# Performance work log

Hardware: AMD Instinct MI355X
Metric: run time of the kernel (lower is better)

The kernel has to match this reference:

```python
import jax, jax.numpy as jnp
import numpy as np

EPS = 1e-8


def setup_inputs() -> dict:
    key = jax.random.key(0)
    ks = jax.random.split(key, 3)
    B, d_in, d_sae = 2048, 2048, 16384
    x = jax.random.normal(ks[0], (B, 2, d_in), dtype=jnp.float32)
    W_enc = jax.random.normal(ks[1], (d_in, d_sae), dtype=jnp.float32) / (d_in ** 0.5)
    W_dec = jax.random.normal(ks[2], (d_sae, d_in), dtype=jnp.float32) / (d_sae ** 0.5)
    b_enc = jnp.zeros((d_sae,), dtype=jnp.float32)
    b_dec = jnp.zeros((d_in,), dtype=jnp.float32)
    return {"x": x, "W_enc": W_enc, "W_dec": W_dec, "b_enc": b_enc,
            "b_dec": b_dec, "k": 64, "h": 8192}


def _encode(x, W_enc, b_enc, k):
    # x: (N, d_in) -> z: (N, d_sae), top-k sparsified with relu on kept values
    pre = x @ W_enc + b_enc
    v, i = jax.lax.top_k(pre, k)                       # (N, k)
    rows = jnp.arange(pre.shape[0])[:, None]
    return jnp.zeros_like(pre).at[rows, i].set(jax.nn.relu(v))


def _info_nce(z_a, z_b):
    z_a = z_a / jnp.maximum(jnp.linalg.norm(z_a, axis=-1, keepdims=True), EPS)
    z_b = z_b / jnp.maximum(jnp.linalg.norm(z_b, axis=-1, keepdims=True), EPS)
    sim = z_a @ z_b.T                                  # (B, B)
    diag = jnp.diagonal(sim)
    ce_row = jnp.mean(jax.nn.logsumexp(sim, axis=1) - diag)
    ce_col = jnp.mean(jax.nn.logsumexp(sim, axis=0) - diag)
    return 0.5 * (ce_row + ce_col)


def reference(x, W_enc, W_dec, b_enc, b_dec, k, h):
    alpha = 1.0
    B, _, d_in = x.shape
    # encode both tokens in one GEMM: (2B, d_in)
    x_flat = x.reshape(B * 2, d_in)
    z = _encode(x_flat, W_enc, b_enc, k)               # (2B, d_sae)
    x_hat_full = z @ W_dec + b_dec                     # (2B, d_in)
    x_hat_high = z[:, :h] @ W_dec[:h, :] + b_dec       # (2B, d_in)
    per_tok = d_in
    # mean over batch per token, summed over prev+cur (matches 4 separate means)
    se_full = jnp.sum((x_hat_full - x_flat) ** 2, axis=-1).reshape(B, 2)
    se_high = jnp.sum((x_hat_high - x_flat) ** 2, axis=-1).reshape(B, 2)
    l_matr = (jnp.mean(se_full, axis=0).sum() + jnp.mean(se_high, axis=0).sum()) / per_tok
    z2 = z.reshape(B, 2, -1)
    z_h_prev = z2[:, 0, :h]
    z_h_cur = z2[:, 1, :h]
    l_contr = _info_nce(z_h_cur, z_h_prev)
    total = l_matr + alpha * l_contr
    x_hat_cur = x_hat_full.reshape(B, 2, d_in)[:, 1]
    z_cur = z2[:, 1]
    return (total, x_hat_cur, z_cur)
```

## Files before the change

kernel.cpp:

```cpp
#include <hip/hip_runtime.h>
#include <hip/hip_bf16.h>
#include <math.h>

#define D_IN   2048
#define D_SAE  16384
#define NROWS  4096
#define KTOP   64
#define HDIM   8192
#define CHUNK  1024
#define EPSN   1e-8f
#define BANDW_F16 4e-3f
#define BANDW_F32 4e-4f
#define BANDCAP 512
#define NTILE   128
#define SEG     16
#define CAPT    (NTILE*SEG)
#define TH_CAND 2.0f

typedef unsigned short u16;
typedef unsigned char u8;
typedef _Float16 f16;
typedef __attribute__((ext_vector_type(8))) _Float16 f16x8;
typedef __attribute__((ext_vector_type(4))) _Float16 f16x4;
typedef __attribute__((ext_vector_type(8))) unsigned short u16x8;
typedef __attribute__((ext_vector_type(4))) float float4v;
typedef __attribute__((ext_vector_type(2))) float f32x2;

__device__ __forceinline__ unsigned f2u(float f) {
  unsigned b = __float_as_uint(f);
  return (b & 0x80000000u) ? ~b : (b | 0x80000000u);
}
__device__ __forceinline__ float u2f(unsigned u) {
  unsigned b = (u & 0x80000000u) ? (u & 0x7fffffffu) : ~u;
  return __uint_as_float(b);
}
__device__ __forceinline__ u16 f2bf_rne(float f) {
  unsigned b = __float_as_uint(f);
  unsigned r = (b + 0x7fffu + ((b >> 16) & 1u)) >> 16;
  return (u16)r;
}
__device__ __forceinline__ float bf2f(u16 u) {
  return __uint_as_float(((unsigned)u) << 16);
}
__device__ __forceinline__ void async_copy16(void* lds, const void* g) {
  __builtin_amdgcn_global_load_lds(
      (const __attribute__((address_space(1))) unsigned*)(g),
      (__attribute__((address_space(3))) unsigned*)(lds), 16, 0, 0);
}

__global__ __launch_bounds__(256)
void pre_kernel(const float* __restrict__ x, const float* __restrict__ W,
                f16* __restrict__ Axh, f16* __restrict__ Th,
                float* __restrict__ WT)
{
  __shared__ float S[64][65];
  const int bid = blockIdx.x;
  if (bid < 8192) {
    const int tx = threadIdx.x & 63, ty = threadIdx.x >> 6;
    const int n0 = (bid & 255) * 64, k0 = (bid >> 8) * 64;
#pragma unroll
    for (int i = 0; i < 16; ++i) {
      int kl = ty + i * 4;
      S[kl][tx] = W[(size_t)(k0 + kl) * D_SAE + n0 + tx];
    }
    __syncthreads();
#pragma unroll
    for (int i = 0; i < 16; ++i) {
      int nl = ty + i * 4;
      float v = S[tx][nl];
      Th[(size_t)(n0 + nl) * D_IN + k0 + tx] = (f16)v;
      WT[(size_t)(n0 + nl) * D_IN + k0 + tx] = v;
    }
  } else {
    int t = (bid - 8192) * 256 + threadIdx.x;
    const int n4 = (NROWS * D_IN) / 4;
    if (t < n4) {
      float4 v = ((const float4*)x)[t];
      f16x4 h;
      h.x = (f16)v.x; h.y = (f16)v.y; h.z = (f16)v.z; h.w = (f16)v.w;
      ((f16x4*)Axh)[t] = h;
    }
  }
}

__global__ __launch_bounds__(256)
void wdec_to_fp8_kernel(const float* __restrict__ W,
                        u8* __restrict__ W8, float* __restrict__ scl)
{
  __shared__ float red[256];
  const int c = blockIdx.x;
  const int tid = threadIdx.x;
  const int e0 = tid * 8;
  const float* wr = W + (size_t)c * 2048;
  float4 a = *(const float4*)(wr + e0);
  float4 b = *(const float4*)(wr + e0 + 4);
  float w[8] = {a.x,a.y,a.z,a.w,b.x,b.y,b.z,b.w};
  float mx = 0.f;
#pragma unroll
  for (int i = 0; i < 8; ++i) mx = fmaxf(mx, fabsf(w[i]));
  red[tid] = mx; __syncthreads();
  for (int s = 128; s > 0; s >>= 1) { if (tid < s) red[tid] = fmaxf(red[tid], red[tid+s]); __syncthreads(); }
  const float mxa = red[0];
  const float senc = mxa > 0.f ? 448.f / mxa : 0.f;
  float q[8];
#pragma unroll
  for (int i = 0; i < 8; ++i) q[i] = fminf(fmaxf(w[i] * senc, -448.f), 448.f);
  int p0 = __builtin_amdgcn_cvt_pk_fp8_f32(q[0], q[1], 0, false);
  p0 = __builtin_amdgcn_cvt_pk_fp8_f32(q[2], q[3], p0, true);
  int p1 = __builtin_amdgcn_cvt_pk_fp8_f32(q[4], q[5], 0, false);
  p1 = __builtin_amdgcn_cvt_pk_fp8_f32(q[6], q[7], p1, true);
  uint2 o; o.x = (unsigned)p0; o.y = (unsigned)p1;
  *(uint2*)(W8 + (size_t)c * 2048 + e0) = o;
  if (tid == 0) scl[c] = mxa > 0.f ? mxa / 448.f : 0.f;
}

__global__ __launch_bounds__(512, 2)
void gemm_f16_kernel(const f16* __restrict__ Axh,
                     const f16* __restrict__ BT,
                     const float* __restrict__ bias,
                     unsigned* __restrict__ ckey_g,
                     u16* __restrict__ cidx_g,
                     unsigned* __restrict__ ccnt)
{
  __shared__ u16 As[2][2][256 * 32];
  __shared__ u16 Bs[2][2][256 * 32];
  const int tid  = threadIdx.x;
  const int wave = tid >> 6, lane = tid & 63;
  const int bid  = blockIdx.x;
  const int xcd  = bid & 7, loc = bid >> 3;
  const int n0   = (xcd * 8 + (loc >> 4)) * 256;
  const int m0   = (loc & 15) * 256;
  const int wr   = wave >> 2;
  const int wc   = wave & 3;
  const int fr   = lane & 15;
  const int fsl  = lane >> 4;

  float4v acc[8][4];
#pragma unroll
  for (int i = 0; i < 8; ++i)
#pragma unroll
    for (int j = 0; j < 4; ++j) acc[i][j] = (float4v){0.f, 0.f, 0.f, 0.f};

  int aoff[8], boff[4];
#pragma unroll
  for (int mi = 0; mi < 8; ++mi) {
    int row = wr * 128 + mi * 16 + fr;
    aoff[mi] = row * 32 + ((fsl ^ ((row >> 1) & 3)) * 8);
  }
#pragma unroll
  for (int n = 0; n < 4; ++n) {
    int col = wc * 64 + n * 16 + fr;
    boff[n] = col * 32 + ((fsl ^ ((col >> 1) & 3)) * 8);
  }

  auto stA = [&](int bf, int tt, int ks, int half) {
    int idx = half * 512 + tid;
    int row = idx >> 2, sl = idx & 3;
    int gc = tt * 64 + ks * 32 + ((sl ^ ((row >> 1) & 3)) * 8);
    async_copy16((char*)&As[bf][ks][0] + (size_t)idx * 16,
                 Axh + (size_t)(m0 + row) * D_IN + gc);
  };
  auto stB = [&](int bf, int tt, int ks, int half) {
    int idx = half * 512 + tid;
    int row = idx >> 2, sl = idx & 3;
    int gc = tt * 64 + ks * 32 + ((sl ^ ((row >> 1) & 3)) * 8);
    async_copy16((char*)&Bs[bf][ks][0] + (size_t)idx * 16,
                 BT + (size_t)(n0 + row) * D_IN + gc);
  };

  stA(0, 0, 0, 0); stA(0, 0, 0, 1); stB(0, 0, 0, 0); stB(0, 0, 0, 1);
  stA(0, 0, 1, 0); stA(0, 0, 1, 1); stB(0, 0, 1, 0); stB(0, 0, 1, 1);
  asm volatile("s_waitcnt vmcnt(4)" ::: "memory");
  __builtin_amdgcn_s_barrier();

  for (int t = 0; t < 32; ++t) {
    const int buf = t & 1, nbf = buf ^ 1;
    const bool st = (t < 31);
#pragma unroll
    for (int ks = 0; ks < 2; ++ks) {
      const u16* Ak = &As[buf][ks][0];
      const u16* Bk = &Bs[buf][ks][0];
      f16x8 b0 = *(const f16x8*)&Bk[boff[0]];
      f16x8 b1 = *(const f16x8*)&Bk[boff[1]];
      f16x8 b2 = *(const f16x8*)&Bk[boff[2]];
      f16x8 b3 = *(const f16x8*)&Bk[boff[3]];
      f16x8 a0 = *(const f16x8*)&Ak[aoff[0]];
      f16x8 a1 = *(const f16x8*)&Ak[aoff[1]];
      f16x8 a2 = *(const f16x8*)&Ak[aoff[2]];
      f16x8 a3 = *(const f16x8*)&Ak[aoff[3]];
      if (st) { stA(nbf, t + 1, ks, 0); stA(nbf, t + 1, ks, 1); }
      __builtin_amdgcn_s_setprio(1);
      acc[0][0] = __builtin_amdgcn_mfma_f32_16x16x32_f16(a0, b0, acc[0][0], 0, 0, 0);
      acc[0][1] = __builtin_amdgcn_mfma_f32_16x16x32_f16(a0, b1, acc[0][1], 0, 0, 0);
      acc[0][2] = __builtin_amdgcn_mfma_f32_16x16x32_f16(a0, b2, acc[0][2], 0, 0, 0);
      acc[0][3] = __builtin_amdgcn_mfma_f32_16x16x32_f16(a0, b3, acc[0][3], 0, 0, 0);
      acc[1][0] = __builtin_amdgcn_mfma_f32_16x16x32_f16(a1, b0, acc[1][0], 0, 0, 0);
      acc[1][1] = __builtin_amdgcn_mfma_f32_16x16x32_f16(a1, b1, acc[1][1], 0, 0, 0);
      acc[1][2] = __builtin_amdgcn_mfma_f32_16x16x32_f16(a1, b2, acc[1][2], 0, 0, 0);
      acc[1][3] = __builtin_amdgcn_mfma_f32_16x16x32_f16(a1, b3, acc[1][3], 0, 0, 0);
      acc[2][0] = __builtin_amdgcn_mfma_f32_16x16x32_f16(a2, b0, acc[2][0], 0, 0, 0);
      acc[2][1] = __builtin_amdgcn_mfma_f32_16x16x32_f16(a2, b1, acc[2][1], 0, 0, 0);
      acc[2][2] = __builtin_amdgcn_mfma_f32_16x16x32_f16(a2, b2, acc[2][2], 0, 0, 0);
      acc[2][3] = __builtin_amdgcn_mfma_f32_16x16x32_f16(a2, b3, acc[2][3], 0, 0, 0);
      acc[3][0] = __builtin_amdgcn_mfma_f32_16x16x32_f16(a3, b0, acc[3][0], 0, 0, 0);
      acc[3][1] = __builtin_amdgcn_mfma_f32_16x16x32_f16(a3, b1, acc[3][1], 0, 0, 0);
      acc[3][2] = __builtin_amdgcn_mfma_f32_16x16x32_f16(a3, b2, acc[3][2], 0, 0, 0);
      acc[3][3] = __builtin_amdgcn_mfma_f32_16x16x32_f16(a3, b3, acc[3][3], 0, 0, 0);
      __builtin_amdgcn_s_setprio(0);
      a0 = *(const f16x8*)&Ak[aoff[4]];
      a1 = *(const f16x8*)&Ak[aoff[5]];
      a2 = *(const f16x8*)&Ak[aoff[6]];
      a3 = *(const f16x8*)&Ak[aoff[7]];
      if (st) { stB(nbf, t + 1, ks, 0); stB(nbf, t + 1, ks, 1); }
      __builtin_amdgcn_s_setprio(1);
      acc[4][0] = __builtin_amdgcn_mfma_f32_16x16x32_f16(a0, b0, acc[4][0], 0, 0, 0);
      acc[4][1] = __builtin_amdgcn_mfma_f32_16x16x32_f16(a0, b1, acc[4][1], 0, 0, 0);
      acc[4][2] = __builtin_amdgcn_mfma_f32_16x16x32_f16(a0, b2, acc[4][2], 0, 0, 0);
      acc[4][3] = __builtin_amdgcn_mfma_f32_16x16x32_f16(a0, b3, acc[4][3], 0, 0, 0);
      acc[5][0] = __builtin_amdgcn_mfma_f32_16x16x32_f16(a1, b0, acc[5][0], 0, 0, 0);
      acc[5][1] = __builtin_amdgcn_mfma_f32_16x16x32_f16(a1, b1, acc[5][1], 0, 0, 0);
      acc[5][2] = __builtin_amdgcn_mfma_f32_16x16x32_f16(a1, b2, acc[5][2], 0, 0, 0);
      acc[5][3] = __builtin_amdgcn_mfma_f32_16x16x32_f16(a1, b3, acc[5][3], 0, 0, 0);
      acc[6][0] = __builtin_amdgcn_mfma_f32_16x16x32_f16(a2, b0, acc[6][0], 0, 0, 0);
      acc[6][1] = __builtin_amdgcn_mfma_f32_16x16x32_f16(a2, b1, acc[6][1], 0, 0, 0);
      acc[6][2] = __builtin_amdgcn_mfma_f32_16x16x32_f16(a2, b2, acc[6][2], 0, 0, 0);
      acc[6][3] = __builtin_amdgcn_mfma_f32_16x16x32_f16(a2, b3, acc[6][3], 0, 0, 0);
      acc[7][0] = __builtin_amdgcn_mfma_f32_16x16x32_f16(a3, b0, acc[7][0], 0, 0, 0);
      acc[7][1] = __builtin_amdgcn_mfma_f32_16x16x32_f16(a3, b1, acc[7][1], 0, 0, 0);
      acc[7][2] = __builtin_amdgcn_mfma_f32_16x16x32_f16(a3, b2, acc[7][2], 0, 0, 0);
      acc[7][3] = __builtin_amdgcn_mfma_f32_16x16x32_f16(a3, b3, acc[7][3], 0, 0, 0);
      __builtin_amdgcn_s_setprio(0);
      if (st) {
        asm volatile("s_waitcnt vmcnt(4)" ::: "memory");
        __builtin_amdgcn_s_barrier();
      } else if (ks == 0) {
        asm volatile("s_waitcnt vmcnt(0)" ::: "memory");
        __builtin_amdgcn_s_barrier();
      }
    }
  }
  __syncthreads();

  unsigned* lcnt = (unsigned*)&As[0][0][0];
  lcnt[tid] = 0u;
  __syncthreads();
  const int tl = wc >> 1;
  const int tileG = (n0 >> 7) + tl;
  const int orow = (lane >> 4) * 4;
#pragma unroll
  for (int mi = 0; mi < 8; ++mi) {
#pragma unroll
    for (int nj = 0; nj < 4; ++nj) {
      int col = n0 + wc * 64 + nj * 16 + fr;
      float bv = bias[col];
#pragma unroll
      for (int rr = 0; rr < 4; ++rr) {
        float val = acc[mi][nj][rr] + bv;
        if (val >= TH_CAND) {
          int lrow = wr * 128 + mi * 16 + orow + rr;
          unsigned j = atomicAdd(&lcnt[tl * 256 + lrow], 1u);
          if (j < SEG) {
            size_t sb = ((size_t)(m0 + lrow) * NTILE + tileG) * SEG;
            ckey_g[sb + j] = f2u(val);
            cidx_g[sb + j] = (u16)col;
          }
        }
      }
    }
  }
  __syncthreads();
  ccnt[(size_t)(m0 + (tid & 255)) * NTILE + (n0 >> 7) + (tid >> 8)] = lcnt[tid];
}

__global__ __launch_bounds__(256)
void select_compact_kernel(const unsigned* __restrict__ ckey_g,
                           const u16* __restrict__ cidx_g,
                           const unsigned* __restrict__ ccnt,
                           const float* __restrict__ x,
                           const float* __restrict__ WT,
                           const float* __restrict__ benc,
                           float bandw,
                           int*   __restrict__ topk_idx,
                           float* __restrict__ topk_val,
                           float* __restrict__ nh_norm,
                           unsigned* __restrict__ flags)
{
  __shared__ unsigned ckey[CAPT];
  __shared__ u16      cidx[CAPT];
  __shared__ unsigned tof[128];
  __shared__ unsigned tc[128];
  __shared__ unsigned hist[256];
  __shared__ unsigned sscan[257];
  __shared__ unsigned wsum[4];
  __shared__ float    bv_l[64];
  __shared__ int      band_idx[BANDCAP];
  __shared__ float    band_val[BANDCAP];
  __shared__ double   band_ex[BANDCAP];
  __shared__ unsigned char picked[BANDCAP];
  __shared__ int      out_idx[64];
  __shared__ float    out_val[64];
  __shared__ float    sh_v64;
  __shared__ unsigned sh_mcnt, sh_bstar, sh_kth, sh_ocnt, sh_bcnt, sh_bad;

  const int tid = threadIdx.x;
  const int wv = tid >> 6, ln = tid & 63;
  const int r = blockIdx.x;

  if (tid == 0) { sh_ocnt = 0u; sh_bcnt = 0u; sh_bad = 0u; sh_mcnt = 0u; sh_bstar = 0xffffffffu; }
  hist[tid] = 0u;
  if (tid < 128) {
    unsigned c = ccnt[(size_t)r * NTILE + tid];
    tc[tid] = c;
    if (c > SEG) sh_bad = 1u;
  }
  __syncthreads();
  if (tid < 128) {
    unsigned v = tc[tid];
#pragma unroll
    for (int d = 1; d < 64; d <<= 1) {
      unsigned t = __shfl_up(v, d);
      if (ln >= d) v += t;
    }
    tof[tid] = v;
  }
  __syncthreads();
  if (tid >= 64 && tid < 128) tof[tid] += tof[63];
  __syncthreads();
  const unsigned cc_u = tof[127];
  const int cc = (int)(cc_u < CAPT ? cc_u : CAPT);

  {
    unsigned ck[8]; u16 ci[8]; unsigned pv[8];
#pragma unroll
    for (int b = 0; b < 8; ++b) {
      int idx = tid + 256 * b;
      int tile = idx >> 4, slot = idx & 15;
      unsigned c = tc[tile]; if (c > SEG) c = SEG;
      bool valid = (unsigned)slot < c;
      pv[b] = valid ? (tof[tile] - tc[tile] + slot) : 0xffffffffu;
      ck[b] = valid ? ckey_g[(size_t)r * CAPT + idx] : 0u;
      ci[b] = valid ? cidx_g[(size_t)r * CAPT + idx] : (u16)0;
    }
#pragma unroll
    for (int b = 0; b < 8; ++b) {
      if (pv[b] < (unsigned)CAPT) { ckey[pv[b]] = ck[b]; cidx[pv[b]] = ci[b]; }
    }
  }
  __syncthreads();

  bool bad = (sh_bad != 0u) || (cc_u < 64u) || (cc_u > (unsigned)CAPT);

  if (!bad) {
    for (int s = tid; s < cc; s += 256) {
      float v = u2f(ckey[s]);
      int b = (int)((v - TH_CAND) * 100.0f);
      b = b < 0 ? 0 : (b > 255 ? 255 : b);
      atomicAdd(&hist[b], 1u);
    }
  }
  __syncthreads();
  {
    int rt = 255 - tid;
    unsigned v = hist[rt];
#pragma unroll
    for (int d = 1; d < 64; d <<= 1) {
      unsigned t = __shfl_up(v, d);
      if (ln >= d) v += t;
    }
    if (ln == 63) wsum[wv] = v;
    __syncthreads();
    unsigned add = 0;
    for (int w = 0; w < wv; ++w) add += wsum[w];
    sscan[rt] = v + add;
    if (tid == 0) sscan[256] = 0u;
    __syncthreads();
    if (sscan[tid] >= 64u && sscan[tid + 1] < 64u) {
      sh_bstar = (unsigned)tid;
      sh_kth = 64u - sscan[tid + 1];
    }
  }
  __syncthreads();

  if (bad || sh_bstar == 0xffffffffu) { if (tid == 0) flags[r] = 1u; return; }
  const int bstar = (int)sh_bstar;
  const unsigned kth = sh_kth;

  for (int s = tid; s < cc; s += 256) {
    float v = u2f(ckey[s]);
    int b = (int)((v - TH_CAND) * 100.0f);
    b = b < 0 ? 0 : (b > 255 ? 255 : b);
    if (b == bstar) {
      unsigned p = atomicAdd(&sh_mcnt, 1u);
      if (p < 64u) bv_l[p] = v;
    }
  }
  __syncthreads();
  if (sh_mcnt > 64u) { if (tid == 0) flags[r] = 1u; return; }
  const int m = (int)sh_mcnt;
  if (wv == 0 && ln < m) {
    float mine = bv_l[ln];
    int rank = 0;
    for (int j = 0; j < m; ++j) {
      float o = bv_l[j];
      if (o > mine || (o == mine && j < ln)) ++rank;
    }
    if (rank == (int)kth - 1) sh_v64 = mine;
  }
  __syncthreads();
  const float v64 = sh_v64;

  const float hi = v64 + 2.f * bandw, lo = v64 - 2.f * bandw;
  for (int s = tid; s < cc; s += 256) {
    float v = u2f(ckey[s]);
    int i = (int)cidx[s];
    if (v > hi) {
      unsigned p = atomicAdd(&sh_ocnt, 1u);
      out_idx[p] = i; out_val[p] = v;
    } else if (v >= lo) {
      unsigned p = atomicAdd(&sh_bcnt, 1u);
      if (p < BANDCAP) { band_idx[p] = i; band_val[p] = v; }
    }
  }
  __syncthreads();
  if (sh_bcnt > BANDCAP) { if (tid == 0) flags[r] = 1u; return; }
  const unsigned nci = sh_ocnt;
  const unsigned bcnt = sh_bcnt;
  const unsigned remaining = 64u - nci;

  if (bcnt == remaining) {
    for (unsigned s = tid; s < bcnt; s += 256) {
      out_idx[nci + s] = band_idx[s];
      out_val[nci + s] = band_val[s];
    }
    __syncthreads();
  } else {
    const float* xr = x + (size_t)r * 2048;
    for (unsigned bi = wv; bi < bcnt; bi += 4) {
      int c = band_idx[bi];
      const float* wr = WT + (size_t)c * 2048;
      double s = 0.0;
      for (int j0 = 0; j0 < 2048; j0 += 512) {
        float xa[8], wa[8];
#pragma unroll
        for (int u = 0; u < 8; ++u) {
          int j = j0 + ln + 64 * u;
          xa[u] = xr[j];
          wa[u] = wr[j];
        }
#pragma unroll
        for (int u = 0; u < 8; ++u)
          s += (double)xa[u] * (double)wa[u];
      }
#pragma unroll
      for (int off2 = 32; off2 > 0; off2 >>= 1)
        s += __shfl_down(s, off2);
      if (ln == 0) band_ex[bi] = s + (double)benc[c];
    }
    __syncthreads();
    if (tid == 0) {
      for (unsigned i2 = 0; i2 < bcnt; ++i2) picked[i2] = 0;
      for (unsigned s = 0; s < remaining; ++s) {
        int best = -1;
        for (unsigned b2 = 0; b2 < bcnt; ++b2) {
          if (picked[b2]) continue;
          if (best < 0 || band_ex[b2] > band_ex[best] ||
              (band_ex[b2] == band_ex[best] && band_idx[b2] < band_idx[best]))
            best = (int)b2;
        }
        picked[best] = 1;
        out_idx[nci + s] = band_idx[best];
        out_val[nci + s] = (float)band_ex[best];
      }
    }
    __syncthreads();
  }

  if (tid < 64) {
    float v = out_val[tid];
    v = v > 0.f ? v : 0.f;
    out_val[tid] = v;
    topk_idx[(size_t)r * 64 + tid] = out_idx[tid];
    topk_val[(size_t)r * 64 + tid] = v;
  }
  __syncthreads();
  if (tid == 0) {
    float n2 = 0.f;
    for (int s = 0; s < 64; ++s)
      if (out_idx[s] < HDIM) n2 += out_val[s] * out_val[s];
    nh_norm[r] = sqrtf(n2);
    flags[r] = 0u;
  }
}

__global__ __launch_bounds__(256)
void repair_kernel(const unsigned* __restrict__ flags,
                   const float* __restrict__ x,
                   const float* __restrict__ WT,
                   const float* __restrict__ benc,
                   int* __restrict__ topk_idx,
                   float* __restrict__ topk_val,
                   float* __restrict__ nh_norm)
{
  const int r = blockIdx.x;
  if (flags[r] == 0u) return;
  __shared__ float prerow[16384];
  __shared__ float xs[2048];
  __shared__ float rv[256];
  __shared__ int   ri[256];
  __shared__ int   oi[64];
  __shared__ float ov[64];
  const int tid = threadIdx.x;
  for (int i = tid; i < 2048; i += 256) xs[i] = x[(size_t)r * 2048 + i];
  __syncthreads();
  for (int c = tid; c < 16384; c += 256) {
    const float* wr = WT + (size_t)c * 2048;
    float s = 0.f;
    for (int j = 0; j < 2048; ++j) s = fmaf(xs[j], wr[j], s);
    prerow[c] = s + benc[c];
  }
  __syncthreads();
  for (int k2 = 0; k2 < 64; ++k2) {
    float bv = -INFINITY; int bi = 16384;
    for (int c = tid; c < 16384; c += 256) {
      float v = prerow[c];
      if (v > bv || (v == bv && c < bi)) { bv = v; bi = c; }
    }
    rv[tid] = bv; ri[tid] = bi;
    __syncthreads();
    for (int s2 = 128; s2 > 0; s2 >>= 1) {
      if (tid < s2) {
        if (rv[tid+s2] > rv[tid] || (rv[tid+s2] == rv[tid] && ri[tid+s2] < ri[tid])) {
          rv[tid] = rv[tid+s2]; ri[tid] = ri[tid+s2];
        }
      }
      __syncthreads();
    }
    if (tid == 0) { oi[k2] = ri[0]; ov[k2] = rv[0]; prerow[ri[0]] = -INFINITY; }
    __syncthreads();
  }
  if (tid < 64) {
    float v = ov[tid]; v = v > 0.f ? v : 0.f;
    topk_idx[(size_t)r * 64 + tid] = oi[tid];
    topk_val[(size_t)r * 64 + tid] = v;
  }
  __syncthreads();
  if (tid == 0) {
    float n2 = 0.f;
    for (int s = 0; s < 64; ++s)
      if (oi[s] < HDIM) { float v = ov[s] > 0.f ? ov[s] : 0.f; n2 += v * v; }
    nh_norm[r] = sqrtf(n2);
  }
}

__global__ __launch_bounds__(256)
void scatter_kernel(const int* __restrict__ topk_idx,
                    const float* __restrict__ topk_val,
                    const float* __restrict__ nh_norm,
                    float* __restrict__ zcur_out,
                    u16* __restrict__ ZpTb)
{
  int t = blockIdx.x * blockDim.x + threadIdx.x;
  if (t >= NROWS * 64) return;
  int r = t >> 6;
  int c = topk_idx[t];
  float v = topk_val[t];
  int b = r >> 1;
  if (r & 1) {
    zcur_out[(size_t)b * 16384 + c] = v;
  } else if (c < HDIM) {
    float nrm = nh_norm[r]; nrm = nrm > EPSN ? nrm : EPSN;
    ZpTb[(size_t)c * 2048 + b] = f2bf_rne(v / nrm);
  }
}

__global__ __launch_bounds__(256)
void token_kernel(const int* __restrict__ topk_idx,
                  const float* __restrict__ topk_val,
                  const u8* __restrict__ W8,
                  const float* __restrict__ scl,
                  const float* __restrict__ bdec,
                  const float* __restrict__ x,
                  const float* __restrict__ nh_norm,
                  const u16* __restrict__ ZpTb,
                  float* __restrict__ se_full,
                  float* __restrict__ se_high,
                  float* __restrict__ xhat_out,
                  float* __restrict__ simb,
                  float* __restrict__ lse_row,
                  float* __restrict__ diag)
{
  __shared__ int sidx[64];
  __shared__ float sval[64];
  __shared__ float red[256];
  __shared__ int cidx2[64];
  __shared__ float cval2[64];
  __shared__ int scnt;
  const int tid = threadIdx.x;
  const int r = blockIdx.x;
  const int e0 = tid * 8;
  if (tid == 0) scnt = 0;
  if (tid < 64) {
    int c = topk_idx[(size_t)r*64+tid];
    sidx[tid] = c;
    sval[tid] = topk_val[(size_t)r*64+tid] * scl[c];
  }
  __syncthreads();
  float accf[8], acch[8];
  {
    float4 b0 = *(const float4*)(bdec + e0);
    float4 b1 = *(const float4*)(bdec + e0 + 4);
    accf[0]=b0.x; accf[1]=b0.y; accf[2]=b0.z; accf[3]=b0.w;
    accf[4]=b1.x; accf[5]=b1.y; accf[6]=b1.z; accf[7]=b1.w;
#pragma unroll
    for (int i = 0; i < 8; ++i) acch[i] = accf[i];
  }
  for (int s0 = 0; s0 < 64; s0 += 8) {
    uint2 w[8]; float vf[8], vh[8];
#pragma unroll
    for (int j = 0; j < 8; ++j) {
      int c = sidx[s0 + j];
      float v = sval[s0 + j];
      vf[j] = v;
      vh[j] = (c < HDIM) ? v : 0.f;
      w[j] = *(const uint2*)(W8 + (size_t)c * 2048 + e0);
    }
#pragma unroll
    for (int j = 0; j < 8; ++j) {
      f32x2 f0 = __builtin_amdgcn_cvt_pk_f32_fp8((int)w[j].x, false);
      f32x2 f1 = __builtin_amdgcn_cvt_pk_f32_fp8((int)w[j].x, true);
      f32x2 f2 = __builtin_amdgcn_cvt_pk_f32_fp8((int)w[j].y, false);
      f32x2 f3 = __builtin_amdgcn_cvt_pk_f32_fp8((int)w[j].y, true);
      float wvv[8] = {f0[0],f0[1],f1[0],f1[1],f2[0],f2[1],f3[0],f3[1]};
#pragma unroll
      for (int i = 0; i < 8; ++i) {
        accf[i] = fmaf(vf[j], wvv[i], accf[i]);
        acch[i] = fmaf(vh[j], wvv[i], acch[i]);
      }
    }
  }
  const float* xr = x + (size_t)r * 2048;
  float4 x0 = *(const float4*)(xr + e0);
  float4 x1 = *(const float4*)(xr + e0 + 4);
  float xv[8] = {x0.x,x0.y,x0.z,x0.w,x1.x,x1.y,x1.z,x1.w};
  float sf = 0.f, shs = 0.f;
#pragma unroll
  for (int i = 0; i < 8; ++i) {
    float df = accf[i] - xv[i]; sf += df*df;
    float dh = acch[i] - xv[i]; shs += dh*dh;
  }
  red[tid] = sf; __syncthreads();
  for (int s2=128; s2>0; s2>>=1){ if (tid<s2) red[tid]+=red[tid+s2]; __syncthreads(); }
  if (tid==0) se_full[r] = red[0];
  __syncthreads();
  red[tid] = shs; __syncthreads();
  for (int s2=128; s2>0; s2>>=1){ if (tid<s2) red[tid]+=red[tid+s2]; __syncthreads(); }
  if (tid==0) se_high[r] = red[0];
  if (!(r & 1)) return;

  {
    float* orow = xhat_out + (size_t)(r >> 1) * 2048;
    float4 o0 = {accf[0],accf[1],accf[2],accf[3]};
    float4 o1 = {accf[4],accf[5],accf[6],accf[7]};
    *(float4*)(orow + e0) = o0;
    *(float4*)(orow + e0 + 4) = o1;
  }
  const int i = r >> 1;
  __syncthreads();
  if (tid < 64) {
    int c = sidx[tid];
    float v = topk_val[(size_t)r*64+tid];
    if (c < HDIM) {
      float nrm = nh_norm[r]; nrm = nrm > EPSN ? nrm : EPSN;
      int p = atomicAdd(&scnt, 1);
      cidx2[p] = c; cval2[p] = v / nrm;
    }
  }
  __syncthreads();
  float acc[8];
#pragma unroll
  for (int ii = 0; ii < 8; ++ii) acc[ii] = 0.f;
  const int m = scnt;
  int s = 0;
  for (; s + 8 <= m; s += 8) {
    u16x8 z[8]; float vv[8];
#pragma unroll
    for (int j = 0; j < 8; ++j) {
      vv[j] = cval2[s + j];
      z[j] = *(const u16x8*)(ZpTb + (size_t)cidx2[s + j] * 2048 + e0);
    }
#pragma unroll
    for (int j = 0; j < 8; ++j)
#pragma unroll
      for (int ii = 0; ii < 8; ++ii)
        acc[ii] = fmaf(vv[j], bf2f(z[j][ii]), acc[ii]);
  }
  for (; s < m; ++s) {
    int c = cidx2[s]; float v = cval2[s];
    u16x8 z8 = *(const u16x8*)(ZpTb + (size_t)c * 2048 + e0);
#pragma unroll
    for (int ii = 0; ii < 8; ++ii)
      acc[ii] = fmaf(v, bf2f(z8[ii]), acc[ii]);
  }
  {
    float* srow = simb + (size_t)i * 2048;
    float4 o0 = {acc[0],acc[1],acc[2],acc[3]};
    float4 o1 = {acc[4],acc[5],acc[6],acc[7]};
    *(float4*)(srow + e0) = o0;
    *(float4*)(srow + e0 + 4) = o1;
  }
  float mx = -INFINITY;
#pragma unroll
  for (int ii = 0; ii < 8; ++ii) mx = fmaxf(mx, acc[ii]);
  if ((i >> 3) == tid) diag[i] = acc[i & 7];
  red[tid] = mx; __syncthreads();
  for (int s2=128; s2>0; s2>>=1){ if (tid<s2) red[tid]=fmaxf(red[tid],red[tid+s2]); __syncthreads(); }
  mx = red[0]; __syncthreads();
  float se = 0.f;
#pragma unroll
  for (int ii = 0; ii < 8; ++ii) se += expf(acc[ii] - mx);
  red[tid] = se; __syncthreads();
  for (int s2=128; s2>0; s2>>=1){ if (tid<s2) red[tid]+=red[tid+s2]; __syncthreads(); }
  if (tid == 0) lse_row[i] = mx + logf(red[0]);
}

__global__ __launch_bounds__(256)
void gemm_pre_kernel(const float* __restrict__ A,
                     const float* __restrict__ B,
                     const float* __restrict__ bias,
                     float* __restrict__ C)
{
  __shared__ float As[16][129];
  __shared__ float Bs[16][129];
  const int tid = threadIdx.x;
  const int tx = tid & 15, ty = tid >> 4;
  const int m0 = blockIdx.y * 128;
  const int n0 = blockIdx.x * 128;
  float acc[8][8];
#pragma unroll
  for (int i = 0; i < 8; ++i)
#pragma unroll
    for (int j = 0; j < 8; ++j) acc[i][j] = 0.f;
  const int lk = tid & 15, lm = tid >> 4;
  for (int k0 = 0; k0 < 2048; k0 += 16) {
#pragma unroll
    for (int i = 0; i < 8; ++i) {
      int m = lm + 16 * i;
      As[lk][m] = A[(size_t)(m0 + m) * 2048 + k0 + lk];
    }
#pragma unroll
    for (int i = 0; i < 8; ++i) {
      int idx = tid + 256 * i;
      int kk = idx >> 7, nn = idx & 127;
      Bs[kk][nn] = B[(size_t)(k0 + kk) * 16384 + n0 + nn];
    }
    __syncthreads();
#pragma unroll
    for (int kk = 0; kk < 16; ++kk) {
      float a[8], b[8];
#pragma unroll
      for (int i = 0; i < 8; ++i) a[i] = As[kk][ty + 16 * i];
#pragma unroll
      for (int j = 0; j < 8; ++j) b[j] = Bs[kk][tx + 16 * j];
#pragma unroll
      for (int i = 0; i < 8; ++i)
#pragma unroll
        for (int j = 0; j < 8; ++j) acc[i][j] = fmaf(a[i], b[j], acc[i][j]);
    }
    __syncthreads();
  }
#pragma unroll
  for (int i = 0; i < 8; ++i) {
    int m = m0 + ty + 16 * i;
#pragma unroll
    for (int j = 0; j < 8; ++j) {
      int n = n0 + tx + 16 * j;
      C[(size_t)m * 16384 + n] = acc[i][j] + bias[n];
    }
  }
}

__global__ __launch_bounds__(256)
void select_fb_kernel(const float* __restrict__ pre,
                      const float* __restrict__ x,
                      const float* __restrict__ Wenc,
                      const float* __restrict__ benc,
                      int row_base, float bandw,
                      int*   __restrict__ topk_idx,
                      float* __restrict__ topk_val,
                      float* __restrict__ nh_norm)
{
  __shared__ unsigned hist[256];
  __shared__ int      band_idx[BANDCAP];
  __shared__ double   band_ex[BANDCAP];
  __shared__ double   red_d[256];
  __shared__ int      out_idx[64];
  __shared__ float    out_val[64];
  __shared__ unsigned char picked[BANDCAP];
  __shared__ unsigned sh_prefix, sh_need, sh_ocnt, sh_bcnt;

  const int tid = threadIdx.x;
  const int lrow = blockIdx.x;
  const int row = row_base + lrow;
  const float* prow = pre + (size_t)lrow * 16384;

  if (tid == 0) { sh_prefix = 0u; sh_need = 64u; }
  __syncthreads();
  for (int level = 24; level >= 0; level -= 8) {
    hist[tid] = 0u;
    __syncthreads();
    unsigned prefix = sh_prefix;
    for (int i = tid; i < 16384; i += 256) {
      unsigned u = f2u(prow[i]);
      bool match = (level == 24) || ((u >> ((level + 8) & 31)) == prefix);
      if (match) atomicAdd(&hist[(u >> level) & 255u], 1u);
    }
    __syncthreads();
    if (tid == 0) {
      unsigned need = sh_need, acc = 0; int q = 0;
      for (int b2 = 255; b2 >= 0; --b2) {
        if (acc + hist[b2] >= need) { q = b2; break; }
        acc += hist[b2];
      }
      sh_prefix = (prefix << 8) | (unsigned)q;
      sh_need = need - acc;
    }
    __syncthreads();
  }
  const float v64 = u2f(sh_prefix);

  if (tid == 0) { sh_ocnt = 0u; sh_bcnt = 0u; }
  __syncthreads();
  const float hi = v64 + 2.f * bandw, lo = v64 - 2.f * bandw;
  for (int i = tid; i < 16384; i += 256) {
    float v = prow[i];
    if (v > hi) {
      unsigned p = atomicAdd(&sh_ocnt, 1u);
      out_idx[p] = i; out_val[p] = v;
    } else if (v >= lo) {
      unsigned p = atomicAdd(&sh_bcnt, 1u);
      if (p < BANDCAP) { band_idx[p] = i; }
    }
  }
  __syncthreads();
  const unsigned nci = sh_ocnt;
  const unsigned bcnt = sh_bcnt < BANDCAP ? sh_bcnt : BANDCAP;
  const unsigned remaining = 64u - nci;

  if (bcnt == remaining) {
    for (unsigned s = tid; s < bcnt; s += 256) {
      int c = band_idx[s];
      out_idx[nci + s] = c;
      out_val[nci + s] = prow[c];
    }
    __syncthreads();
  } else {
    const float* xr = x + (size_t)row * 2048;
    for (unsigned bi = 0; bi < bcnt; ++bi) {
      int c = band_idx[bi];
      double part = 0.0;
#pragma unroll
      for (int j2 = 0; j2 < 8; ++j2) {
        int kk = tid + 256 * j2;
        part += (double)xr[kk] * (double)Wenc[(size_t)kk * 16384 + c];
      }
      red_d[tid] = part;
      __syncthreads();
      for (int sft = 128; sft > 0; sft >>= 1) {
        if (tid < sft) red_d[tid] += red_d[tid + sft];
        __syncthreads();
      }
      if (tid == 0) band_ex[bi] = red_d[0] + (double)benc[c];
      __syncthreads();
    }
    if (tid == 0) {
      for (unsigned i2 = 0; i2 < bcnt; ++i2) picked[i2] = 0;
      for (unsigned s = 0; s < remaining; ++s) {
        int best = -1;
        for (unsigned b2 = 0; b2 < bcnt; ++b2) {
          if (picked[b2]) continue;
          if (best < 0 || band_ex[b2] > band_ex[best] ||
              (band_ex[b2] == band_ex[best] && band_idx[b2] < band_idx[best]))
            best = (int)b2;
        }
        picked[best] = 1;
        out_idx[nci + s] = band_idx[best];
        out_val[nci + s] = (float)band_ex[best];
      }
    }
    __syncthreads();
  }

  if (tid < 64) {
    float v = out_val[tid];
    v = v > 0.f ? v : 0.f;
    out_val[tid] = v;
    topk_idx[(size_t)row * 64 + tid] = out_idx[tid];
    topk_val[(size_t)row * 64 + tid] = v;
  }
  __syncthreads();
  if (tid == 0) {
    float n2 = 0.f;
    for (int s = 0; s < 64; ++s)
      if (out_idx[s] < HDIM) n2 += out_val[s] * out_val[s];
    nh_norm[row] = sqrtf(n2);
  }
}

__global__ __launch_bounds__(256)
void scatter_f32_kernel(const int* __restrict__ topk_idx,
                        const float* __restrict__ topk_val,
                        const float* __restrict__ nh_norm,
                        float* __restrict__ zcur_out,
                        float* __restrict__ ZpT)
{
  int t = blockIdx.x * blockDim.x + threadIdx.x;
  if (t >= NROWS * 64) return;
  int r = t >> 6;
  int c = topk_idx[t];
  float v = topk_val[t];
  int b = r >> 1;
  if (r & 1) {
    zcur_out[(size_t)b * 16384 + c] = v;
  } else if (c < HDIM) {
    float nrm = nh_norm[r]; nrm = nrm > EPSN ? nrm : EPSN;
    ZpT[(size_t)c * 2048 + b] = v / nrm;
  }
}

__global__ __launch_bounds__(256)
void decode_f32_kernel(const int* __restrict__ topk_idx,
                       const float* __restrict__ topk_val,
                       const float* __restrict__ Wdec,
                       const float* __restrict__ bdec,
                       const float* __restrict__ x,
                       float* __restrict__ se_full,
                       float* __restrict__ se_high,
                       float* __restrict__ xhat_out)
{
  __shared__ int sidx[64];
  __shared__ float sval[64];
  __shared__ float red[256];
  const int tid = threadIdx.x;
  const int r = blockIdx.x;
  if (tid < 64) { sidx[tid] = topk_idx[(size_t)r*64+tid]; sval[tid] = topk_val[(size_t)r*64+tid]; }
  __syncthreads();
  float accf[8], acch[8];
#pragma unroll
  for (int i = 0; i < 8; ++i) { float b = bdec[tid + 256*i]; accf[i] = b; acch[i] = b; }
  for (int s = 0; s < 64; ++s) {
    int c = sidx[s]; float v = sval[s];
    const float* wr = Wdec + (size_t)c * 2048;
    bool high = (c < HDIM);
#pragma unroll
    for (int i = 0; i < 8; ++i) {
      float w = wr[tid + 256*i];
      accf[i] = fmaf(v, w, accf[i]);
      if (high) acch[i] = fmaf(v, w, acch[i]);
    }
  }
  const float* xr = x + (size_t)r * 2048;
  float sf = 0.f, shs = 0.f;
#pragma unroll
  for (int i = 0; i < 8; ++i) {
    float xv = xr[tid + 256*i];
    float df = accf[i] - xv; sf += df*df;
    float dh = acch[i] - xv; shs += dh*dh;
  }
  red[tid] = sf; __syncthreads();
  for (int s2=128; s2>0; s2>>=1){ if (tid<s2) red[tid]+=red[tid+s2]; __syncthreads(); }
  if (tid==0) se_full[r] = red[0];
  __syncthreads();
  red[tid] = shs; __syncthreads();
  for (int s2=128; s2>0; s2>>=1){ if (tid<s2) red[tid]+=red[tid+s2]; __syncthreads(); }
  if (tid==0) se_high[r] = red[0];
  if (r & 1) {
    float* orow = xhat_out + (size_t)(r >> 1) * 2048;
#pragma unroll
    for (int i = 0; i < 8; ++i) orow[tid + 256*i] = accf[i];
  }
}

__global__ __launch_bounds__(256)
void sim_f32_kernel(const int* __restrict__ topk_idx,
                    const float* __restrict__ topk_val,
                    const float* __restrict__ nh_norm,
                    const float* __restrict__ ZpT,
                    float* __restrict__ sim)
{
  __shared__ int cidx2[64];
  __shared__ float cval2[64];
  __shared__ int scnt;
  const int tid = threadIdx.x;
  const int i = blockIdx.x;
  const int r = 2 * i + 1;
  if (tid == 0) scnt = 0;
  __syncthreads();
  if (tid < 64) {
    int c = topk_idx[(size_t)r*64+tid];
    float v = topk_val[(size_t)r*64+tid];
    if (c < HDIM) {
      float nrm = nh_norm[r]; nrm = nrm > EPSN ? nrm : EPSN;
      int p = atomicAdd(&scnt, 1);
      cidx2[p] = c; cval2[p] = v / nrm;
    }
  }
  __syncthreads();
  float acc[8];
#pragma unroll
  for (int ii = 0; ii < 8; ++ii) acc[ii] = 0.f;
  int m = scnt;
  for (int s = 0; s < m; ++s) {
    int c = cidx2[s]; float v = cval2[s];
    const float* zr = ZpT + (size_t)c * 2048;
#pragma unroll
    for (int ii = 0; ii < 8; ++ii)
      acc[ii] = fmaf(v, zr[tid + 256*ii], acc[ii]);
  }
  float* srow = sim + (size_t)i * 2048;
#pragma unroll
  for (int ii = 0; ii < 8; ++ii) srow[tid + 256*ii] = acc[ii];
}

__global__ __launch_bounds__(256)
void lse_row_kernel(const float* __restrict__ sim,
                    float* __restrict__ lse_row, float* __restrict__ diag)
{
  __shared__ float red[256];
  const int tid = threadIdx.x; const int i = blockIdx.x;
  const int e0 = tid * 8;
  const float* srow = sim + (size_t)i * 2048;
  float4 v0 = *(const float4*)(srow + e0);
  float4 v1 = *(const float4*)(srow + e0 + 4);
  float vals[8] = {v0.x,v0.y,v0.z,v0.w,v1.x,v1.y,v1.z,v1.w};
  float mx = -INFINITY;
#pragma unroll
  for (int ii=0; ii<8; ++ii) mx = fmaxf(mx, vals[ii]);
  if ((i >> 3) == tid) diag[i] = vals[i & 7];
  red[tid]=mx; __syncthreads();
  for (int s=128;s>0;s>>=1){ if (tid<s) red[tid]=fmaxf(red[tid],red[tid+s]); __syncthreads(); }
  mx = red[0]; __syncthreads();
  float se=0.f;
#pragma unroll
  for (int ii=0;ii<8;++ii) se += expf(vals[ii]-mx);
  red[tid]=se; __syncthreads();
  for (int s=128;s>0;s>>=1){ if (tid<s) red[tid]+=red[tid+s]; __syncthreads(); }
  if (tid==0) lse_row[i] = mx + logf(red[0]);
}

__global__ __launch_bounds__(256)
void lse_col_kernel(const float* __restrict__ sim, float* __restrict__ lse_col)
{
  __shared__ float ml[32][9], sl[32][9];
  const int tid = threadIdx.x;
  const int c = tid & 7, rr = tid >> 3;
  const int col = blockIdx.x * 8 + c;
  float m = -INFINITY, s = 0.f;
  for (int r = rr; r < 2048; r += 32) {
    float v = sim[(size_t)r * 2048 + col];
    float mn = fmaxf(m, v);
    s = s * expf(m - mn) + expf(v - mn);
    m = mn;
  }
  ml[rr][c] = m; sl[rr][c] = s;
  __syncthreads();
  if (rr == 0) {
    float M = ml[0][c];
#pragma unroll
    for (int i = 1; i < 32; ++i) M = fmaxf(M, ml[i][c]);
    float S = 0.f;
#pragma unroll
    for (int i = 0; i < 32; ++i) S += sl[i][c] * expf(ml[i][c] - M);
    lse_col[col] = M + logf(S);
  }
}

__global__ __launch_bounds__(256)
void final_kernel(const float* __restrict__ se_full, const float* __restrict__ se_high,
                  const float* __restrict__ lse_row, const float* __restrict__ lse_col,
                  const float* __restrict__ diag, float* __restrict__ out0)
{
  __shared__ float red[256];
  const int tid = threadIdx.x;
  float s1 = 0.f;
  for (int i = tid; i < 4096; i += 256) s1 += se_full[i] + se_high[i];
  red[tid]=s1; __syncthreads();
  for (int s=128;s>0;s>>=1){ if (tid<s) red[tid]+=red[tid+s]; __syncthreads(); }
  float matr = red[0]; __syncthreads();
  float s2 = 0.f;
  for (int i = tid; i < 2048; i += 256) s2 += (lse_row[i]-diag[i]) + (lse_col[i]-diag[i]);
  red[tid]=s2; __syncthreads();
  for (int s=128;s>0;s>>=1){ if (tid<s) red[tid]+=red[tid+s]; __syncthreads(); }
  if (tid == 0) {
    float l_matr  = matr / (2048.f * 2048.f);
    float l_contr = 0.5f * (red[0] / 2048.f);
    out0[0] = l_matr + l_contr;
  }
}

extern "C" void kernel_launch(void* const* d_in, const int* in_sizes, int n_in,
                              void* d_out, int out_size, void* d_ws, size_t ws_size,
                              hipStream_t stream)
{
  const float* x    = (const float*)d_in[0];
  const float* Wenc = (const float*)d_in[1];
  const float* Wdec = (const float*)d_in[2];
  const float* benc = (const float*)d_in[3];
  const float* bdec = (const float*)d_in[4];
  float* out = (float*)d_out;
  float* xhat_out = out + 1;
  float* zcur_out = out + 1 + (size_t)2048 * 2048;
  (void)in_sizes; (void)n_in; (void)out_size;

  char* ws = (char*)d_ws;
  size_t off = 0;
  auto alloc = [&](size_t bytes) {
    char* p = ws + off; off += (bytes + 255) & ~(size_t)255; return p;
  };
  int*      tki     = (int*)     alloc((size_t)NROWS * 64 * 4);
  float*    tkv     = (float*)   alloc((size_t)NROWS * 64 * 4);
  float*    nh_norm = (float*)   alloc((size_t)NROWS * 4);
  float*    se_f    = (float*)   alloc((size_t)NROWS * 4);
  float*    se_h    = (float*)   alloc((size_t)NROWS * 4);
  float*    lse_r   = (float*)   alloc((size_t)2048 * 4);
  float*    lse_c   = (float*)   alloc((size_t)2048 * 4);
  float*    diag    = (float*)   alloc((size_t)2048 * 4);
  f16*      Axh     = (f16*)     alloc((size_t)NROWS * D_IN * 2);
  unsigned* ckey_g  = (unsigned*)alloc((size_t)NROWS * CAPT * 4);
  u16*      cidx_g  = (u16*)     alloc((size_t)NROWS * CAPT * 2);
  unsigned* ccnt    = (unsigned*)alloc((size_t)NROWS * NTILE * 4);
  unsigned* flags   = (unsigned*)alloc((size_t)NROWS * 4);
  char*     R1      = alloc((size_t)D_SAE * D_IN * 2);
  char*     R2      = alloc((size_t)D_SAE * D_IN * 4);
  size_t need = off;

  f16*   Th    = (f16*)R1;
  u8*    W8    = (u8*)R1;
  float* scl   = (float*)(R1 + (size_t)D_SAE * D_IN);
  float* WT    = (float*)R2;
  u16*   ZpTb  = (u16*)R2;
  float* simb  = (float*)(R2 + (size_t)8192 * 2048 * 2);

  hipMemsetAsync(zcur_out, 0, (size_t)2048 * 16384 * 4, stream);

  if (ws_size >= need) {
    pre_kernel<<<16384, 256, 0, stream>>>(x, Wenc, Axh, Th, WT);
    gemm_f16_kernel<<<1024, 512, 0, stream>>>(Axh, Th, benc, ckey_g, cidx_g, ccnt);
    select_compact_kernel<<<NROWS, 256, 0, stream>>>(ckey_g, cidx_g, ccnt, x, WT, benc,
        BANDW_F16, tki, tkv, nh_norm, flags);
    repair_kernel<<<NROWS, 256, 0, stream>>>(flags, x, WT, benc, tki, tkv, nh_norm);
    wdec_to_fp8_kernel<<<D_SAE, 256, 0, stream>>>(Wdec, W8, scl);
    hipMemsetAsync(ZpTb, 0, (size_t)8192 * 2048 * 2, stream);
    scatter_kernel<<<(NROWS * 64) / 256, 256, 0, stream>>>(tki, tkv, nh_norm, zcur_out, ZpTb);
    token_kernel<<<NROWS, 256, 0, stream>>>(tki, tkv, W8, scl, bdec, x, nh_norm, ZpTb,
        se_f, se_h, xhat_out, simb, lse_r, diag);
    lse_col_kernel<<<256, 256, 0, stream>>>(simb, lse_c);
    final_kernel<<<1, 256, 0, stream>>>(se_f, se_h, lse_r, lse_c, diag, out);
  } else {
    off = 0;
    float* pre2  = (float*)alloc((size_t)CHUNK * 16384 * 4);
    int*   tki2  = (int*)  alloc((size_t)NROWS * 64 * 4);
    float* tkv2  = (float*)alloc((size_t)NROWS * 64 * 4);
    float* nh2   = (float*)alloc((size_t)NROWS * 4);
    float* sef2  = (float*)alloc((size_t)NROWS * 4);
    float* seh2  = (float*)alloc((size_t)NROWS * 4);
    float* lr2   = (float*)alloc((size_t)2048 * 4);
    float* lc2   = (float*)alloc((size_t)2048 * 4);
    float* dg2   = (float*)alloc((size_t)2048 * 4);
    float* ZpT2  = (float*)alloc((size_t)8192 * 2048 * 4);
    float* sim2  = (float*)alloc((size_t)2048 * 2048 * 4);
    for (int ch = 0; ch < 4; ++ch) {
      dim3 g(128, 8);
      gemm_pre_kernel<<<g, 256, 0, stream>>>(x + (size_t)ch * CHUNK * 2048, Wenc, benc, pre2);
      select_fb_kernel<<<CHUNK, 256, 0, stream>>>(pre2, x, Wenc, benc,
          ch * CHUNK, BANDW_F32, tki2, tkv2, nh2);
    }
    hipMemsetAsync(ZpT2, 0, (size_t)8192 * 2048 * 4, stream);
    scatter_f32_kernel<<<(NROWS * 64) / 256, 256, 0, stream>>>(tki2, tkv2, nh2, zcur_out, ZpT2);
    decode_f32_kernel<<<NROWS, 256, 0, stream>>>(tki2, tkv2, Wdec, bdec, x, sef2, seh2, xhat_out);
    sim_f32_kernel<<<2048, 256, 0, stream>>>(tki2, tkv2, nh2, ZpT2, sim2);
    lse_row_kernel<<<2048, 256, 0, stream>>>(sim2, lr2, dg2);
    lse_col_kernel<<<256, 256, 0, stream>>>(sim2, lc2);
    final_kernel<<<1, 256, 0, stream>>>(sef2, seh2, lr2, lc2, dg2, out);
  }
}
```

Baseline: 696.7 us.

## Write dense z_cur rows in token kernel and fuse fp8 conversion with scatter

Drops the 128MB memset of the z_cur output and the separate scatter pass. Each odd-row token block now writes its full dense z_cur row, built from a 16KB shared-memory index map. The W_dec fp8 conversion and the ZpTb scatter for even rows are merged into one launch. This saves a full extra write pass over the output and one kernel launch, at the cost of 16KB more LDS per token block, which may lower occupancy, and the dense row write now sits inside the token kernel.

Result: no change. 684.8 us (-1.7%).

```diff
diff --git a/kernel.cpp b/kernel.cpp
--- a/kernel.cpp
+++ b/kernel.cpp
@@ -81,37 +81,6 @@
       ((f16x4*)Axh)[t] = h;
     }
   }
-}
-
-__global__ __launch_bounds__(256)
-void wdec_to_fp8_kernel(const float* __restrict__ W,
-                        u8* __restrict__ W8, float* __restrict__ scl)
-{
-  __shared__ float red[256];
-  const int c = blockIdx.x;
-  const int tid = threadIdx.x;
-  const int e0 = tid * 8;
-  const float* wr = W + (size_t)c * 2048;
-  float4 a = *(const float4*)(wr + e0);
-  float4 b = *(const float4*)(wr + e0 + 4);
-  float w[8] = {a.x,a.y,a.z,a.w,b.x,b.y,b.z,b.w};
-  float mx = 0.f;
-#pragma unroll
-  for (int i = 0; i < 8; ++i) mx = fmaxf(mx, fabsf(w[i]));
-  red[tid] = mx; __syncthreads();
-  for (int s = 128; s > 0; s >>= 1) { if (tid < s) red[tid] = fmaxf(red[tid], red[tid+s]); __syncthreads(); }
-  const float mxa = red[0];
-  const float senc = mxa > 0.f ? 448.f / mxa : 0.f;
-  float q[8];
-#pragma unroll
-  for (int i = 0; i < 8; ++i) q[i] = fminf(fmaxf(w[i] * senc, -448.f), 448.f);
-  int p0 = __builtin_amdgcn_cvt_pk_fp8_f32(q[0], q[1], 0, false);
-  p0 = __builtin_amdgcn_cvt_pk_fp8_f32(q[2], q[3], p0, true);
-  int p1 = __builtin_amdgcn_cvt_pk_fp8_f32(q[4], q[5], 0, false);
-  p1 = __builtin_amdgcn_cvt_pk_fp8_f32(q[6], q[7], p1, true);
-  uint2 o; o.x = (unsigned)p0; o.y = (unsigned)p1;
-  *(uint2*)(W8 + (size_t)c * 2048 + e0) = o;
-  if (tid == 0) scl[c] = mxa > 0.f ? mxa / 448.f : 0.f;
 }
 
 __global__ __launch_bounds__(512, 2)
@@ -553,23 +522,52 @@
 }
 
 __global__ __launch_bounds__(256)
-void scatter_kernel(const int* __restrict__ topk_idx,
-                    const float* __restrict__ topk_val,
-                    const float* __restrict__ nh_norm,
-                    float* __restrict__ zcur_out,
-                    u16* __restrict__ ZpTb)
-{
-  int t = blockIdx.x * blockDim.x + threadIdx.x;
-  if (t >= NROWS * 64) return;
-  int r = t >> 6;
-  int c = topk_idx[t];
-  float v = topk_val[t];
-  int b = r >> 1;
-  if (r & 1) {
-    zcur_out[(size_t)b * 16384 + c] = v;
-  } else if (c < HDIM) {
-    float nrm = nh_norm[r]; nrm = nrm > EPSN ? nrm : EPSN;
-    ZpTb[(size_t)c * 2048 + b] = f2bf_rne(v / nrm);
+void wdec_scatter_kernel(const float* __restrict__ W,
+                         u8* __restrict__ W8, float* __restrict__ scl,
+                         const int* __restrict__ topk_idx,
+                         const float* __restrict__ topk_val,
+                         const float* __restrict__ nh_norm,
+                         u16* __restrict__ ZpTb)
+{
+  const int bid = blockIdx.x;
+  const int tid = threadIdx.x;
+  if (bid < 16384) {
+    __shared__ float red[256];
+    const int c = bid;
+    const int e0 = tid * 8;
+    const float* wr = W + (size_t)c * 2048;
+    float4 a = *(const float4*)(wr + e0);
+    float4 b = *(const float4*)(wr + e0 + 4);
+    float w[8] = {a.x,a.y,a.z,a.w,b.x,b.y,b.z,b.w};
+    float mx = 0.f;
+#pragma unroll
+    for (int i = 0; i < 8; ++i) mx = fmaxf(mx, fabsf(w[i]));
+    red[tid] = mx; __syncthreads();
+    for (int s = 128; s > 0; s >>= 1) { if (tid < s) red[tid] = fmaxf(red[tid], red[tid+s]); __syncthreads(); }
+    const float mxa = red[0];
+    const float senc = mxa > 0.f ? 448.f / mxa : 0.f;
+    float q[8];
+#pragma unroll
+    for (int i = 0; i < 8; ++i) q[i] = fminf(fmaxf(w[i] * senc, -448.f), 448.f);
+    int p0 = __builtin_amdgcn_cvt_pk_fp8_f32(q[0], q[1], 0, false);
+    p0 = __builtin_amdgcn_cvt_pk_fp8_f32(q[2], q[3], p0, true);
+    int p1 = __builtin_amdgcn_cvt_pk_fp8_f32(q[4], q[5], 0, false);
+    p1 = __builtin_amdgcn_cvt_pk_fp8_f32(q[6], q[7], p1, true);
+    uint2 o; o.x = (unsigned)p0; o.y = (unsigned)p1;
+    *(uint2*)(W8 + (size_t)c * 2048 + e0) = o;
+    if (tid == 0) scl[c] = mxa > 0.f ? mxa / 448.f : 0.f;
+  } else {
+    int t = (bid - 16384) * 256 + tid;
+    if (t < 2048 * 64) {
+      int b = t >> 6;
+      int r = 2 * b;
+      int c = topk_idx[(size_t)r * 64 + (t & 63)];
+      float v = topk_val[(size_t)r * 64 + (t & 63)];
+      if (c < HDIM) {
+        float nrm = nh_norm[r]; nrm = nrm > EPSN ? nrm : EPSN;
+        ZpTb[(size_t)c * 2048 + b] = f2bf_rne(v / nrm);
+      }
+    }
   }
 }
 
@@ -585,26 +583,38 @@
                   float* __restrict__ se_full,
                   float* __restrict__ se_high,
                   float* __restrict__ xhat_out,
+                  float* __restrict__ zcur_out,
                   float* __restrict__ simb,
                   float* __restrict__ lse_row,
                   float* __restrict__ diag)
 {
   __shared__ int sidx[64];
   __shared__ float sval[64];
+  __shared__ float rawv[64];
   __shared__ float red[256];
   __shared__ int cidx2[64];
   __shared__ float cval2[64];
+  __shared__ u8 zmap[16384];
   __shared__ int scnt;
   const int tid = threadIdx.x;
   const int r = blockIdx.x;
   const int e0 = tid * 8;
+  const bool odd = (r & 1);
   if (tid == 0) scnt = 0;
+  if (odd) {
+    unsigned* zm = (unsigned*)zmap;
+#pragma unroll
+    for (int j = 0; j < 16; ++j) zm[tid + 256 * j] = 0xFFFFFFFFu;
+  }
   if (tid < 64) {
     int c = topk_idx[(size_t)r*64+tid];
+    float v = topk_val[(size_t)r*64+tid];
     sidx[tid] = c;
-    sval[tid] = topk_val[(size_t)r*64+tid] * scl[c];
-  }
-  __syncthreads();
+    rawv[tid] = v;
+    sval[tid] = v * scl[c];
+  }
+  __syncthreads();
+  if (odd && tid < 64) zmap[sidx[tid]] = (u8)tid;
   float accf[8], acch[8];
   {
     float4 b0 = *(const float4*)(bdec + e0);
@@ -655,7 +665,7 @@
   red[tid] = shs; __syncthreads();
   for (int s2=128; s2>0; s2>>=1){ if (tid<s2) red[tid]+=red[tid+s2]; __syncthreads(); }
   if (tid==0) se_high[r] = red[0];
-  if (!(r & 1)) return;
+  if (!odd) return;
 
   {
     float* orow = xhat_out + (size_t)(r >> 1) * 2048;
@@ -664,11 +674,24 @@
     *(float4*)(orow + e0) = o0;
     *(float4*)(orow + e0 + 4) = o1;
   }
+  {
+    float* zrow = zcur_out + (size_t)(r >> 1) * 16384;
+#pragma unroll
+    for (int it = 0; it < 16; ++it) {
+      int c0 = it * 1024 + tid * 4;
+      float4 o;
+      u8 s0m = zmap[c0 + 0]; o.x = (s0m < 64) ? rawv[s0m] : 0.f;
+      u8 s1m = zmap[c0 + 1]; o.y = (s1m < 64) ? rawv[s1m] : 0.f;
+      u8 s2m = zmap[c0 + 2]; o.z = (s2m < 64) ? rawv[s2m] : 0.f;
+      u8 s3m = zmap[c0 + 3]; o.w = (s3m < 64) ? rawv[s3m] : 0.f;
+      *(float4*)(zrow + c0) = o;
+    }
+  }
   const int i = r >> 1;
   __syncthreads();
   if (tid < 64) {
     int c = sidx[tid];
-    float v = topk_val[(size_t)r*64+tid];
+    float v = rawv[tid];
     if (c < HDIM) {
       float nrm = nh_norm[r]; nrm = nrm > EPSN ? nrm : EPSN;
       int p = atomicAdd(&scnt, 1);
@@ -1140,19 +1163,17 @@
   u16*   ZpTb  = (u16*)R2;
   float* simb  = (float*)(R2 + (size_t)8192 * 2048 * 2);
 
-  hipMemsetAsync(zcur_out, 0, (size_t)2048 * 16384 * 4, stream);
-
   if (ws_size >= need) {
     pre_kernel<<<16384, 256, 0, stream>>>(x, Wenc, Axh, Th, WT);
     gemm_f16_kernel<<<1024, 512, 0, stream>>>(Axh, Th, benc, ckey_g, cidx_g, ccnt);
     select_compact_kernel<<<NROWS, 256, 0, stream>>>(ckey_g, cidx_g, ccnt, x, WT, benc,
         BANDW_F16, tki, tkv, nh_norm, flags);
     repair_kernel<<<NROWS, 256, 0, stream>>>(flags, x, WT, benc, tki, tkv, nh_norm);
-    wdec_to_fp8_kernel<<<D_SAE, 256, 0, stream>>>(Wdec, W8, scl);
     hipMemsetAsync(ZpTb, 0, (size_t)8192 * 2048 * 2, stream);
-    scatter_kernel<<<(NROWS * 64) / 256, 256, 0, stream>>>(tki, tkv, nh_norm, zcur_out, ZpTb);
+    wdec_scatter_kernel<<<16384 + 512, 256, 0, stream>>>(Wdec, W8, scl,
+        tki, tkv, nh_norm, ZpTb);
     token_kernel<<<NROWS, 256, 0, stream>>>(tki, tkv, W8, scl, bdec, x, nh_norm, ZpTb,
-        se_f, se_h, xhat_out, simb, lse_r, diag);
+        se_f, se_h, xhat_out, zcur_out, simb, lse_r, diag);
     lse_col_kernel<<<256, 256, 0, stream>>>(simb, lse_c);
     final_kernel<<<1, 256, 0, stream>>>(se_f, se_h, lse_r, lse_c, diag, out);
   } else {
@@ -1168,6 +1189,7 @@
     float* dg2   = (float*)alloc((size_t)2048 * 4);
     float* ZpT2  = (float*)alloc((size_t)8192 * 2048 * 4);
     float* sim2  = (float*)alloc((size_t)2048 * 2048 * 4);
+    hipMemsetAsync(zcur_out, 0, (size_t)2048 * 16384 * 4, stream);
     for (int ch = 0; ch < 4; ++ch) {
       dim3 g(128, 8);
       gemm_pre_kernel<<<g, 256, 0, stream>>>(x + (size_t)ch * CHUNK * 2048, Wenc, benc, pre2);
```
